# Kernel tuning notes

Measured on AMD Instinct MI355X. Metric: run time of the kernel, lower is better.

The kernel has to match this reference:

```python
import jax, jax.numpy as jnp
import numpy as np

B, T, D, U = 64, 512, 1024, 128


def setup_inputs() -> dict:
    key = jax.random.key(0)
    ks = jax.random.split(key, 6)
    inputs = jax.random.normal(ks[0], (B, T, D), dtype=jnp.float32)
    # left-aligned boolean mask from random sequence lengths in [T//2, T]
    lengths = jax.random.randint(ks[1], (B,), T // 2, T + 1)
    mask = jnp.arange(T)[None, :] < lengths[:, None]  # [B, T] bool
    kernel = jax.random.normal(ks[2], (D, U), dtype=jnp.float32) / np.sqrt(D).astype(np.float32)
    bias = jnp.zeros((U,), dtype=jnp.float32)
    chain_kernel = jax.random.normal(ks[3], (U, U), dtype=jnp.float32) * 0.1
    # boundary_initializer='zeros' in the module; use small randn so the path is exercised
    left_boundary = jax.random.normal(ks[4], (U,), dtype=jnp.float32) * 0.1
    right_boundary = jax.random.normal(ks[5], (U,), dtype=jnp.float32) * 0.1
    return dict(inputs=inputs, mask=mask, kernel=kernel, bias=bias,
                chain_kernel=chain_kernel, left_boundary=left_boundary,
                right_boundary=right_boundary)


def _add_boundary_energy(potentials, mask, start, end):
    # start energy where mask turns on, end energy where mask turns off (tfa semantics)
    right_shift = jnp.pad(mask[:, :-1], ((0, 0), (1, 0)))  # mask shifted right by 1
    left_shift = jnp.pad(mask[:, 1:], ((0, 0), (0, 1)))    # mask shifted left by 1
    start_mask = (mask & ~right_shift)[..., None].astype(potentials.dtype)  # [B,T,1]
    end_mask = (mask & ~left_shift)[..., None].astype(potentials.dtype)     # [B,T,1]
    return potentials + start_mask * start[None, None, :] + end_mask * end[None, None, :]


def _viterbi_decode(potentials, chain_kernel, mask):
    # potentials: [B,T,U], chain_kernel: [U,U], mask: [B,T] bool (left-aligned)
    Uz = potentials.shape[-1]
    iota = jnp.arange(Uz)

    def fwd_step(state, xs):
        pot_t, m_t = xs                                    # [B,U], [B]
        scores = state[:, :, None] + chain_kernel[None]    # [B,U_prev,U_next]
        bp = jnp.argmax(scores, axis=1)                    # [B,U]
        new_state = pot_t + jnp.max(scores, axis=1)        # [B,U]
        m = m_t[:, None]
        state = jnp.where(m, new_state, state)             # carry state past padding
        bp = jnp.where(m, bp, iota[None, :])               # identity backpointer on padding
        return state, bp

    init = potentials[:, 0]
    xs = (jnp.swapaxes(potentials[:, 1:], 0, 1), mask[:, 1:].T)
    final_state, bps = jax.lax.scan(fwd_step, init, xs)    # bps: [T-1,B,U]
    last_tag = jnp.argmax(final_state, axis=-1)            # [B]

    def back_step(tag, bp):
        prev = jnp.take_along_axis(bp, tag[:, None], axis=1)[:, 0]
        return prev, tag

    first_tag, tags_rest = jax.lax.scan(back_step, last_tag, bps, reverse=True)
    return jnp.concatenate([first_tag[:, None], tags_rest.T], axis=1)  # [B,T] int32


def reference(inputs, mask, kernel, bias, chain_kernel, left_boundary, right_boundary):
    # unary potentials via the internal Dense(units) (use_kernel=True)
    potentials = jnp.einsum('btd,du->btu', inputs, kernel) + bias
    # boundary energies (use_boundary=True)
    potentials = _add_boundary_energy(potentials, mask, left_boundary, right_boundary)
    # Viterbi decode (predict-phase output), one-hot as in the wrapper layer
    tags = _viterbi_decode(potentials, chain_kernel, mask)
    decoded_onehot = jax.nn.one_hot(tags, potentials.shape[-1], dtype=potentials.dtype)
    # train phase returns potentials, predict phase returns the one-hot decode;
    # return both so either path can be checked
    return potentials, decoded_onehot
```

## Files before the change

### kernel.cpp

```cpp
#include <hip/hip_runtime.h>
#include <cstdint>
#include <cstddef>

#define BB 64
#define TT 512
#define DD 1024
#define UU 128
#define MM (BB*TT)

#define WAVE_SYNC() do { asm volatile("s_waitcnt lgkmcnt(0)" ::: "memory"); \
                         __builtin_amdgcn_s_barrier(); } while (0)

__device__ __forceinline__ int mask_elem_bytes(const uint8_t* m) {
    return m[1] ? 1 : 4;
}
__device__ __forceinline__ int mask_at(const uint8_t* m, int eb, int idx) {
    return m[(size_t)idx * eb] != 0;
}

#define BM 64
#define KC 32

__global__ __launch_bounds__(256) void gemm_pot(
    const float* __restrict__ A, const float* __restrict__ Bw,
    const float* __restrict__ bias, const float* __restrict__ lb,
    const float* __restrict__ rb, const uint8_t* __restrict__ mask,
    float* __restrict__ out)
{
    __shared__ float As[KC][68];
    __shared__ float Bs[KC][132];

    const int tid = threadIdx.x;
    const int m0  = blockIdx.x * BM;
    const int rg  = tid >> 5;
    const int cg  = tid & 31;

    const int s_kg  = tid & 7;
    const int s_row = tid >> 3;
    const int b_c4  = tid & 31;
    const int b_kr0 = tid >> 5;

    float acc[8][4];
    #pragma unroll
    for (int r = 0; r < 8; ++r)
        #pragma unroll
        for (int e = 0; e < 4; ++e) acc[r][e] = 0.f;

    const float* aptr0 = A + (size_t)(m0 + s_row)      * DD + s_kg * 4;
    const float* aptr1 = A + (size_t)(m0 + s_row + 32) * DD + s_kg * 4;

    float4 a_pre0 = *(const float4*)(aptr0);
    float4 a_pre1 = *(const float4*)(aptr1);
    float4 b_pre[4];
    #pragma unroll
    for (int p = 0; p < 4; ++p)
        b_pre[p] = *(const float4*)(Bw + (size_t)(b_kr0 + p*8) * UU + b_c4*4);

    for (int k0 = 0; k0 < DD; k0 += KC) {
        __syncthreads();
        {
            const float av0[4] = {a_pre0.x, a_pre0.y, a_pre0.z, a_pre0.w};
            const float av1[4] = {a_pre1.x, a_pre1.y, a_pre1.z, a_pre1.w};
            #pragma unroll
            for (int e = 0; e < 4; ++e) {
                As[s_kg*4 + e][s_row]      = av0[e];
                As[s_kg*4 + e][s_row + 32] = av1[e];
            }
            #pragma unroll
            for (int p = 0; p < 4; ++p)
                *(float4*)&Bs[b_kr0 + p*8][b_c4*4] = b_pre[p];
        }
        __syncthreads();

        if (k0 + KC < DD) {
            a_pre0 = *(const float4*)(aptr0 + k0 + KC);
            a_pre1 = *(const float4*)(aptr1 + k0 + KC);
            #pragma unroll
            for (int p = 0; p < 4; ++p)
                b_pre[p] = *(const float4*)(Bw + (size_t)(k0 + KC + b_kr0 + p*8) * UU + b_c4*4);
        }

        #pragma unroll
        for (int kk = 0; kk < KC; ++kk) {
            float4 b4  = *(const float4*)&Bs[kk][cg*4];
            float4 a40 = *(const float4*)&As[kk][rg*8];
            float4 a41 = *(const float4*)&As[kk][rg*8 + 4];
            const float av[8] = {a40.x, a40.y, a40.z, a40.w, a41.x, a41.y, a41.z, a41.w};
            #pragma unroll
            for (int r = 0; r < 8; ++r) {
                acc[r][0] = fmaf(av[r], b4.x, acc[r][0]);
                acc[r][1] = fmaf(av[r], b4.y, acc[r][1]);
                acc[r][2] = fmaf(av[r], b4.z, acc[r][2]);
                acc[r][3] = fmaf(av[r], b4.w, acc[r][3]);
            }
        }
    }

    const float4 bias4 = *(const float4*)&bias[cg*4];
    const float4 lb4   = *(const float4*)&lb[cg*4];
    const float4 rb4   = *(const float4*)&rb[cg*4];
    const int eb = mask_elem_bytes(mask);

    #pragma unroll
    for (int r = 0; r < 8; ++r) {
        const int m  = m0 + rg*8 + r;
        const int bi = m >> 9;
        const int ti = m & 511;
        const int mt = mask_at(mask, eb, bi*TT + ti);
        const int mp = (ti > 0)      ? mask_at(mask, eb, bi*TT + ti - 1) : 0;
        const int mn = (ti < TT - 1) ? mask_at(mask, eb, bi*TT + ti + 1) : 0;
        const float sflag = (mt && !mp) ? 1.f : 0.f;
        const float eflag = (mt && !mn) ? 1.f : 0.f;
        float4 o;
        o.x = acc[r][0] + bias4.x + sflag*lb4.x + eflag*rb4.x;
        o.y = acc[r][1] + bias4.y + sflag*lb4.y + eflag*rb4.y;
        o.z = acc[r][2] + bias4.z + sflag*lb4.z + eflag*rb4.z;
        o.w = acc[r][3] + bias4.w + sflag*lb4.w + eflag*rb4.w;
        *(float4*)&out[(size_t)m*UU + cg*4] = o;
    }
}

template<bool STORE_MX>
__global__ __launch_bounds__(512) void viterbi_fwd(
    const float* __restrict__ pot, const uint8_t* __restrict__ mask,
    const float* __restrict__ chain, float* __restrict__ hist,
    float* __restrict__ mxb)
{
    const int b   = blockIdx.x;
    const int tid = threadIdx.x;
    const int w   = tid >> 6;
    const int l   = tid & 63;
    const int seg = tid >> 7;
    const int j   = tid & 127;

    __shared__ float st[8][2][128];
    __shared__ float part[2][4][132];
    __shared__ int   wcnt[8];

    const int eb = mask_elem_bytes(mask);
    const int mm = mask_at(mask, eb, b*TT + tid);
    const unsigned long long bal = __ballot(mm);
    if (l == 0) wcnt[w] = __popcll(bal);

    float cc[32];
    #pragma unroll
    for (int k = 0; k < 32; ++k) cc[k] = chain[(seg*32 + k)*UU + j];

    const float* Pb = pot + (size_t)b*TT*UU;
    float* Hb = hist + (size_t)b*TT*UU;
    float* Xb = STORE_MX ? (mxb + (size_t)b*TT*UU) : nullptr;

    {
        const float p0 = Pb[l], p1 = Pb[l + 64];
        st[w][0][l] = p0; st[w][0][l + 64] = p1;
        if (w == 0) { Hb[l] = p0; Hb[l + 64] = p1; }
    }
    float potc0 = Pb[(size_t)UU + l], potc1 = Pb[(size_t)UU + l + 64];
    __syncthreads();

    int len = 0;
    #pragma unroll
    for (int q = 0; q < 8; ++q) len += wcnt[q];

    for (int t = 1; t < len; ++t) {
        const int cur = (t - 1) & 1;

        float a0 = -3.4e38f, a1 = a0;
        const float4* sp = (const float4*)&st[w][cur][seg*32];
        #pragma unroll
        for (int q = 0; q < 8; ++q) {
            const float4 s4 = sp[q];
            const float t0 = s4.x + cc[4*q + 0];
            const float t1 = s4.y + cc[4*q + 1];
            const float t2 = s4.z + cc[4*q + 2];
            const float t3 = s4.w + cc[4*q + 3];
            a0 = fmaxf(fmaxf(a0, t0), t1);
            a1 = fmaxf(fmaxf(a1, t2), t3);
        }
        part[cur][seg][j] = fmaxf(a0, a1);

        float pn0 = 0.f, pn1 = 0.f;
        if (t + 1 < len) {
            pn0 = Pb[(size_t)(t + 1)*UU + l];
            pn1 = Pb[(size_t)(t + 1)*UU + l + 64];
        }

        WAVE_SYNC();

        const float m0 = fmaxf(fmaxf(fmaxf(part[cur][0][l],      part[cur][1][l]),
                                     part[cur][2][l]),      part[cur][3][l]);
        const float m1 = fmaxf(fmaxf(fmaxf(part[cur][0][l + 64], part[cur][1][l + 64]),
                                     part[cur][2][l + 64]), part[cur][3][l + 64]);
        const float ns0 = potc0 + m0;
        const float ns1 = potc1 + m1;
        st[w][cur ^ 1][l]      = ns0;
        st[w][cur ^ 1][l + 64] = ns1;
        if (w == 0) {
            Hb[(size_t)t*UU + l]      = ns0;
            Hb[(size_t)t*UU + l + 64] = ns1;
            if (STORE_MX) {
                Xb[(size_t)t*UU + l]      = m0;
                Xb[(size_t)t*UU + l + 64] = m1;
            }
        }
        potc0 = pn0; potc1 = pn1;
    }
}

__global__ __launch_bounds__(64) void viterbi_bt_eq(
    const float* __restrict__ hist, const float* __restrict__ mxb,
    const uint8_t* __restrict__ mask, const float* __restrict__ chain,
    float* __restrict__ oh)
{
    const int b = blockIdx.x;
    const int l = threadIdx.x;

    __shared__ float ct[128][128];
    for (int r = 0; r < 256; ++r) {
        const int idx = r*64 + l;
        const int i = idx >> 7;
        const int j = idx & 127;
        ct[j][(i + j) & 127] = chain[i*UU + j];
    }

    const int eb = mask_elem_bytes(mask);
    int cnt = 0;
    #pragma unroll
    for (int e = 0; e < 8; ++e) cnt += mask_at(mask, eb, b*TT + e*64 + l);
    #pragma unroll
    for (int off = 32; off > 0; off >>= 1) cnt += __shfl_down(cnt, off);
    const int len = __shfl(cnt, 0);
    __syncthreads();

    const float* Hb = hist + (size_t)b*TT*UU;
    const float* Xb = mxb  + (size_t)b*TT*UU;

    const float v0 = Hb[(size_t)(len-1)*UU + l], v1 = Hb[(size_t)(len-1)*UU + l + 64];
    float mx = fmaxf(v0, v1);
    #pragma unroll
    for (int off = 32; off > 0; off >>= 1) mx = fmaxf(mx, __shfl_xor(mx, off));
    const unsigned long long c0 = __ballot(v0 == mx);
    const unsigned long long c1 = __ballot(v1 == mx);
    int tag = c0 ? __builtin_ctzll(c0) : 64 + __builtin_ctzll(c1);

    for (int t = len + l; t < TT; t += 64)
        oh[((size_t)b*TT + t)*UU + tag] = 1.0f;

    const int r2 = (len >= 2) ? len - 2 : 0;
    const int r3 = (len >= 3) ? len - 3 : 0;
    float hc0 = Hb[(size_t)r2*UU + l], hc1 = Hb[(size_t)r2*UU + l + 64];
    float hm0 = Hb[(size_t)r3*UU + l], hm1 = Hb[(size_t)r3*UU + l + 64];
    float xc0 = Xb[(size_t)(len-1)*UU + l], xc1 = Xb[(size_t)(len-1)*UU + l + 64];
    float xm0 = Xb[(size_t)r2*UU + l],      xm1 = Xb[(size_t)r2*UU + l + 64];

    for (int t = len - 1; t >= 1; --t) {
        if (l == 0) oh[((size_t)b*TT + t)*UU + tag] = 1.0f;

        const int th = (t >= 3) ? t - 3 : 0;
        const int tx = (t >= 2) ? t - 2 : 0;
        const float hf0 = Hb[(size_t)th*UU + l], hf1 = Hb[(size_t)th*UU + l + 64];
        const float xf0 = Xb[(size_t)tx*UU + l], xf1 = Xb[(size_t)tx*UU + l + 64];

        const float Va = __shfl(xc0, tag & 63);
        const float Vb = __shfl(xc1, tag & 63);
        const float V  = (tag < 64) ? Va : Vb;

        const float w0 = hc0 + ct[tag][(l + tag) & 127];
        const float w1 = hc1 + ct[tag][(l + 64 + tag) & 127];
        const unsigned long long b0 = __ballot(w0 == V);
        const unsigned long long b1 = __ballot(w1 == V);
        if (b0)      tag = __builtin_ctzll(b0);
        else if (b1) tag = 64 + __builtin_ctzll(b1);

        hc0 = hm0; hc1 = hm1; hm0 = hf0; hm1 = hf1;
        xc0 = xm0; xc1 = xm1; xm0 = xf0; xm1 = xf1;
    }
    if (l == 0) oh[((size_t)b*TT)*UU + tag] = 1.0f;
}

__global__ __launch_bounds__(64) void viterbi_bt(
    const float* __restrict__ hist, const uint8_t* __restrict__ mask,
    const float* __restrict__ chain, float* __restrict__ oh)
{
    const int b = blockIdx.x;
    const int l = threadIdx.x;

    __shared__ float ct[128][128];
    for (int r = 0; r < 256; ++r) {
        const int idx = r*64 + l;
        const int i = idx >> 7;
        const int j = idx & 127;
        ct[j][(i + j) & 127] = chain[i*UU + j];
    }

    const int eb = mask_elem_bytes(mask);
    int cnt = 0;
    #pragma unroll
    for (int e = 0; e < 8; ++e) cnt += mask_at(mask, eb, b*TT + e*64 + l);
    #pragma unroll
    for (int off = 32; off > 0; off >>= 1) cnt += __shfl_down(cnt, off);
    const int len = __shfl(cnt, 0);
    __syncthreads();

    const float* srow = &hist[((size_t)b*TT + (len - 1))*UU];
    const float v0 = srow[l], v1 = srow[l + 64];
    float mx = fmaxf(v0, v1);
    #pragma unroll
    for (int off = 32; off > 0; off >>= 1) mx = fmaxf(mx, __shfl_xor(mx, off));
    const unsigned long long c0 = __ballot(v0 == mx);
    const unsigned long long c1 = __ballot(v1 == mx);
    int tag = c0 ? __builtin_ctzll(c0) : 64 + __builtin_ctzll(c1);

    for (int t = len + l; t < TT; t += 64)
        oh[((size_t)b*TT + t)*UU + tag] = 1.0f;

    for (int t = len - 1; t >= 1; --t) {
        if (l == 0) oh[((size_t)b*TT + t)*UU + tag] = 1.0f;
        const float* sr = &hist[((size_t)b*TT + (t - 1))*UU];
        const float s0 = sr[l], s1 = sr[l + 64];
        const float w0 = s0 + ct[tag][(l + tag) & 127];
        const float w1 = s1 + ct[tag][(l + 64 + tag) & 127];
        float m2 = fmaxf(w0, w1);
        #pragma unroll
        for (int off = 32; off > 0; off >>= 1) m2 = fmaxf(m2, __shfl_xor(m2, off));
        const unsigned long long b0 = __ballot(w0 == m2);
        const unsigned long long b1 = __ballot(w1 == m2);
        tag = b0 ? __builtin_ctzll(b0) : 64 + __builtin_ctzll(b1);
    }
    if (l == 0) oh[((size_t)b*TT)*UU + tag] = 1.0f;
}

extern "C" void kernel_launch(void* const* d_in, const int* in_sizes, int n_in,
                              void* d_out, int out_size, void* d_ws, size_t ws_size,
                              hipStream_t stream)
{
    (void)in_sizes; (void)n_in; (void)out_size;
    const float*   inp   = (const float*)d_in[0];
    const uint8_t* mask  = (const uint8_t*)d_in[1];
    const float*   kern  = (const float*)d_in[2];
    const float*   bias  = (const float*)d_in[3];
    const float*   chain = (const float*)d_in[4];
    const float*   lb    = (const float*)d_in[5];
    const float*   rb    = (const float*)d_in[6];

    const size_t nel = (size_t)BB*TT*UU;
    float* pot  = (float*)d_out;
    float* oh   = pot + nel;
    float* hist = (float*)d_ws;
    float* mxb  = hist + nel;
    const bool eq_path = ws_size >= 2 * nel * sizeof(float);

    hipMemsetAsync(oh, 0, nel*sizeof(float), stream);
    gemm_pot<<<MM/BM, 256, 0, stream>>>(inp, kern, bias, lb, rb, mask, pot);
    if (eq_path) {
        viterbi_fwd<true><<<BB, 512, 0, stream>>>(pot, mask, chain, hist, mxb);
        viterbi_bt_eq<<<BB, 64, 0, stream>>>(hist, mxb, mask, chain, oh);
    } else {
        viterbi_fwd<false><<<BB, 512, 0, stream>>>(pot, mask, chain, hist, nullptr);
        viterbi_bt<<<BB, 64, 0, stream>>>(hist, mask, chain, oh);
    }
}
```

Measured before the change: 704.4 us.

## Halve Viterbi forward block size with single shared state and wave-0 reduction

Shrinks the forward Viterbi kernel from 8 to 4 waves; each wave now computes partial maxima for all 128 next states over a 32-row slice of the previous state. Instead of every wave redundantly maintaining its own copy of the state, wave 0 alone reduces the partials, writes the shared state and history, and prefetches potentials two steps ahead. This reduces redundant work and register/LDS footprint but adds a second block barrier per time step and serializes the reduction onto one wave.

Result: slower. 774.5 us (+10.0%).

```diff
diff --git a/kernel.cpp b/kernel.cpp
--- a/kernel.cpp
+++ b/kernel.cpp
@@ -121,7 +121,7 @@
 }
 
 template<bool STORE_MX>
-__global__ __launch_bounds__(512) void viterbi_fwd(
+__global__ __launch_bounds__(256) void viterbi_fwd(
     const float* __restrict__ pot, const uint8_t* __restrict__ mask,
     const float* __restrict__ chain, float* __restrict__ hist,
     float* __restrict__ mxb)
@@ -130,80 +130,86 @@
     const int tid = threadIdx.x;
     const int w   = tid >> 6;
     const int l   = tid & 63;
-    const int seg = tid >> 7;
-    const int j   = tid & 127;
-
-    __shared__ float st[8][2][128];
-    __shared__ float part[2][4][132];
-    __shared__ int   wcnt[8];
+
+    __shared__ float st[2][128];
+    __shared__ float part[4][132];
+    __shared__ int   wcnt[4];
 
     const int eb = mask_elem_bytes(mask);
-    const int mm = mask_at(mask, eb, b*TT + tid);
-    const unsigned long long bal = __ballot(mm);
-    if (l == 0) wcnt[w] = __popcll(bal);
-
-    float cc[32];
-    #pragma unroll
-    for (int k = 0; k < 32; ++k) cc[k] = chain[(seg*32 + k)*UU + j];
+    const int ma = mask_at(mask, eb, b*TT + tid);
+    const int mb = mask_at(mask, eb, b*TT + 256 + tid);
+    const unsigned long long bal1 = __ballot(ma);
+    const unsigned long long bal2 = __ballot(mb);
+    if (l == 0) wcnt[w] = __popcll(bal1) + __popcll(bal2);
+
+    float ccL[32], ccH[32];
+    #pragma unroll
+    for (int k = 0; k < 32; ++k) {
+        ccL[k] = chain[(w*32 + k)*UU + l];
+        ccH[k] = chain[(w*32 + k)*UU + l + 64];
+    }
 
     const float* Pb = pot + (size_t)b*TT*UU;
     float* Hb = hist + (size_t)b*TT*UU;
     float* Xb = STORE_MX ? (mxb + (size_t)b*TT*UU) : nullptr;
 
-    {
+    float potc0 = 0.f, potc1 = 0.f, pn0 = 0.f, pn1 = 0.f;
+    if (w == 0) {
         const float p0 = Pb[l], p1 = Pb[l + 64];
-        st[w][0][l] = p0; st[w][0][l + 64] = p1;
-        if (w == 0) { Hb[l] = p0; Hb[l + 64] = p1; }
-    }
-    float potc0 = Pb[(size_t)UU + l], potc1 = Pb[(size_t)UU + l + 64];
+        st[0][l] = p0; st[0][l + 64] = p1;
+        Hb[l] = p0; Hb[l + 64] = p1;
+        potc0 = Pb[(size_t)UU + l];   potc1 = Pb[(size_t)UU + l + 64];
+        pn0   = Pb[(size_t)2*UU + l]; pn1   = Pb[(size_t)2*UU + l + 64];
+    }
     __syncthreads();
 
-    int len = 0;
-    #pragma unroll
-    for (int q = 0; q < 8; ++q) len += wcnt[q];
+    const int len = wcnt[0] + wcnt[1] + wcnt[2] + wcnt[3];
 
     for (int t = 1; t < len; ++t) {
         const int cur = (t - 1) & 1;
 
-        float a0 = -3.4e38f, a1 = a0;
-        const float4* sp = (const float4*)&st[w][cur][seg*32];
+        const float4* sp = (const float4*)&st[cur][w*32];
+        float aL = -3.4e38f, aH = -3.4e38f;
         #pragma unroll
         for (int q = 0; q < 8; ++q) {
             const float4 s4 = sp[q];
-            const float t0 = s4.x + cc[4*q + 0];
-            const float t1 = s4.y + cc[4*q + 1];
-            const float t2 = s4.z + cc[4*q + 2];
-            const float t3 = s4.w + cc[4*q + 3];
-            a0 = fmaxf(fmaxf(a0, t0), t1);
-            a1 = fmaxf(fmaxf(a1, t2), t3);
-        }
-        part[cur][seg][j] = fmaxf(a0, a1);
-
-        float pn0 = 0.f, pn1 = 0.f;
-        if (t + 1 < len) {
-            pn0 = Pb[(size_t)(t + 1)*UU + l];
-            pn1 = Pb[(size_t)(t + 1)*UU + l + 64];
+            aL = fmaxf(fmaxf(aL, s4.x + ccL[4*q + 0]), s4.y + ccL[4*q + 1]);
+            aL = fmaxf(fmaxf(aL, s4.z + ccL[4*q + 2]), s4.w + ccL[4*q + 3]);
+            aH = fmaxf(fmaxf(aH, s4.x + ccH[4*q + 0]), s4.y + ccH[4*q + 1]);
+            aH = fmaxf(fmaxf(aH, s4.z + ccH[4*q + 2]), s4.w + ccH[4*q + 3]);
+        }
+        part[w][l]      = aL;
+        part[w][l + 64] = aH;
+
+        float q0 = 0.f, q1 = 0.f;
+        if (w == 0) {
+            const int tn = (t + 2 < TT) ? (t + 2) : (TT - 1);
+            q0 = Pb[(size_t)tn*UU + l];
+            q1 = Pb[(size_t)tn*UU + l + 64];
         }
 
         WAVE_SYNC();
 
-        const float m0 = fmaxf(fmaxf(fmaxf(part[cur][0][l],      part[cur][1][l]),
-                                     part[cur][2][l]),      part[cur][3][l]);
-        const float m1 = fmaxf(fmaxf(fmaxf(part[cur][0][l + 64], part[cur][1][l + 64]),
-                                     part[cur][2][l + 64]), part[cur][3][l + 64]);
-        const float ns0 = potc0 + m0;
-        const float ns1 = potc1 + m1;
-        st[w][cur ^ 1][l]      = ns0;
-        st[w][cur ^ 1][l + 64] = ns1;
         if (w == 0) {
+            const float m0 = fmaxf(fmaxf(fmaxf(part[0][l],      part[1][l]),
+                                         part[2][l]),      part[3][l]);
+            const float m1 = fmaxf(fmaxf(fmaxf(part[0][l + 64], part[1][l + 64]),
+                                         part[2][l + 64]), part[3][l + 64]);
+            const float ns0 = potc0 + m0;
+            const float ns1 = potc1 + m1;
+            st[cur ^ 1][l]      = ns0;
+            st[cur ^ 1][l + 64] = ns1;
             Hb[(size_t)t*UU + l]      = ns0;
             Hb[(size_t)t*UU + l + 64] = ns1;
             if (STORE_MX) {
                 Xb[(size_t)t*UU + l]      = m0;
                 Xb[(size_t)t*UU + l + 64] = m1;
             }
-        }
-        potc0 = pn0; potc1 = pn1;
+            potc0 = pn0; potc1 = pn1;
+            pn0 = q0;    pn1 = q1;
+        }
+
+        WAVE_SYNC();
     }
 }
 
@@ -353,10 +359,10 @@
     hipMemsetAsync(oh, 0, nel*sizeof(float), stream);
     gemm_pot<<<MM/BM, 256, 0, stream>>>(inp, kern, bias, lb, rb, mask, pot);
     if (eq_path) {
-        viterbi_fwd<true><<<BB, 512, 0, stream>>>(pot, mask, chain, hist, mxb);
+        viterbi_fwd<true><<<BB, 256, 0, stream>>>(pot, mask, chain, hist, mxb);
         viterbi_bt_eq<<<BB, 64, 0, stream>>>(hist, mxb, mask, chain, oh);
     } else {
-        viterbi_fwd<false><<<BB, 512, 0, stream>>>(pot, mask, chain, hist, nullptr);
+        viterbi_fwd<false><<<BB, 256, 0, stream>>>(pot, mask, chain, hist, nullptr);
         viterbi_bt<<<BB, 64, 0, stream>>>(hist, mask, chain, oh);
     }
 }
```
